# Optimization experiments

Hardware: AMD Instinct MI355X
Metric: run time of the kernel (lower is better)

## Reference

```python
import jax, jax.numpy as jnp
import numpy as np
import math

N_EXP = 8
TOP_K = 2
CAPACITY_FACTOR = 1.25


def _capacity(num_tokens):
    cap = math.floor(TOP_K * CAPACITY_FACTOR * num_tokens / N_EXP)
    cap += cap % 2  # round up to even, as in nanoMoE
    return int(cap)


def setup_inputs() -> dict:
    key = jax.random.key(0)
    k1, k2, k3, k4 = jax.random.split(key, 4)
    B, C, d = 4, 1024, 1024
    x = jax.random.normal(k1, (B, C, d), dtype=jnp.float32)
    w_g = jax.random.normal(k2, (d, N_EXP), dtype=jnp.float32) * 0.02
    c_fc = jax.random.normal(k3, (N_EXP, d, 4 * d), dtype=jnp.float32) * 0.02
    c_proj = jax.random.normal(k4, (N_EXP, 4 * d, d), dtype=jnp.float32) * 0.02
    return {"x": x, "w_g": w_g, "c_fc": c_fc, "c_proj": c_proj}


def reference(x, w_g, c_fc, c_proj):
    B, C, d = x.shape
    T = B * C  # num_tokens (static)
    cap = _capacity(T)
    xt = x.reshape(T, d)

    # ---- Router (no noise: use_noisy_top_k=False, eval) ----
    logits = xt @ w_g                                   # [T, n_exp]
    top_v, top_i = jax.lax.top_k(logits, TOP_K)         # [T, k]
    full = jnp.full_like(logits, -jnp.inf)
    full = full.at[jnp.arange(T)[:, None], top_i].set(top_v)
    probs = jax.nn.softmax(full, axis=-1)               # [T, n_exp]

    # expert assignment mask and intra-expert rank (capacity dropping)
    exp_mask = jax.nn.one_hot(top_i, N_EXP, dtype=jnp.int32)       # [T, k, n_exp]
    exp_mask = jnp.transpose(exp_mask, (1, 0, 2))                  # [k, T, n_exp]
    exp_rank = jnp.cumsum(exp_mask.reshape(TOP_K * T, N_EXP), axis=0) - 1
    exp_rank = exp_rank.reshape(TOP_K, T, N_EXP)
    exp_mask = exp_mask * (exp_rank < cap).astype(jnp.int32)       # drop overflow
    exp_rank = jnp.sum(exp_mask * exp_rank, axis=-1)               # [k, T] slot id

    exp_weights = exp_mask.astype(x.dtype) * probs[None]           # [k, T, n_exp]
    rank_oh = jax.nn.one_hot(exp_rank, cap, dtype=x.dtype)         # [k, T, cap]
    # dense combine weights [T, n_exp, cap] (as in original code)
    cb_weight = jnp.einsum('kte,ktc->tec', exp_weights, rank_oh)
    sec_mask = (cb_weight != 0).astype(x.dtype)                    # dispatch mask

    # dispatch tokens into per-expert batches [n_exp, cap, d]
    exp_batches = jnp.einsum('tec,td->ecd', sec_mask, xt)

    # ---- MLPExperts: batched GEMM -> GELU (exact) -> batched GEMM ----
    h = jax.nn.gelu(jnp.einsum('ecd,edf->ecf', exp_batches, c_fc), approximate=False)
    exp_out = jnp.einsum('ecf,efd->ecd', h, c_proj)                # [n_exp, cap, d]

    # ---- weighted combine: [T, n_exp*cap] @ [n_exp*cap, d] ----
    out = cb_weight.reshape(T, N_EXP * cap) @ exp_out.reshape(N_EXP * cap, d)
    return out.reshape(B, C, d)
```

## Files before the change

kernel.cpp:

```cpp
#include <hip/hip_runtime.h>
#include <hip/hip_bf16.h>
#include <math.h>

#define T_TOK 4096
#define D     1024
#define DFF   4096
#define NEXP  8
#define CAP   1280
#define TOPK  2

typedef __bf16 bf16x8 __attribute__((ext_vector_type(8)));
typedef float floatx4 __attribute__((ext_vector_type(4)));

__device__ __forceinline__ unsigned short f2bf(float f) {
  union { float f; unsigned u; } un; un.f = f;
  unsigned r = un.u + 0x7FFF + ((un.u >> 16) & 1);
  return (unsigned short)(r >> 16);
}

__global__ __launch_bounds__(256) void router_kernel(
    const float* __restrict__ x, const float* __restrict__ wg,
    int* __restrict__ top_e, float* __restrict__ top_p) {
  int t = blockIdx.x * 4 + (threadIdx.x >> 6);
  int lane = threadIdx.x & 63;
  if (t >= T_TOK) return;
  const float* xr = x + (size_t)t * D;
  float acc[NEXP];
#pragma unroll
  for (int e = 0; e < NEXP; e++) acc[e] = 0.f;
  for (int dd = lane; dd < D; dd += 64) {
    float xv = xr[dd];
    const float* wr = wg + dd * NEXP;
#pragma unroll
    for (int e = 0; e < NEXP; e++) acc[e] += xv * wr[e];
  }
#pragma unroll
  for (int off = 32; off > 0; off >>= 1) {
#pragma unroll
    for (int e = 0; e < NEXP; e++) acc[e] += __shfl_xor(acc[e], off, 64);
  }
  if (lane == 0) {
    int b0 = 0; float v0 = acc[0];
    for (int e = 1; e < NEXP; e++) if (acc[e] > v0) { v0 = acc[e]; b0 = e; }
    int b1 = -1; float v1 = -INFINITY;
    for (int e = 0; e < NEXP; e++) if (e != b0 && acc[e] > v1) { v1 = acc[e]; b1 = e; }
    float e1 = expf(v1 - v0);
    float s = 1.0f + e1;
    top_e[t * 2 + 0] = b0; top_e[t * 2 + 1] = b1;
    top_p[t * 2 + 0] = 1.0f / s; top_p[t * 2 + 1] = e1 / s;
  }
}

__global__ __launch_bounds__(1024) void rank_kernel(
    const int* __restrict__ top_e, const float* __restrict__ top_p,
    int* __restrict__ slot_token, int* __restrict__ tok_slot,
    float* __restrict__ tok_w) {
  __shared__ int wsum[16][NEXP];
  __shared__ int wscan[16][NEXP];
  int tid = threadIdx.x;
  int lane = tid & 63, w = tid >> 6;

  for (int s = tid; s < NEXP * CAP; s += 1024) slot_token[s] = -1;
  __syncthreads();

  int base[NEXP];
#pragma unroll
  for (int e = 0; e < NEXP; e++) base[e] = 0;

  for (int k = 0; k < TOPK; k++) {
    int cnt[NEXP];
#pragma unroll
    for (int e = 0; e < NEXP; e++) cnt[e] = 0;
    int eloc[4];
#pragma unroll
    for (int i = 0; i < 4; i++) {
      int t = tid * 4 + i;
      int e = top_e[t * 2 + k];
      eloc[i] = e;
#pragma unroll
      for (int q = 0; q < NEXP; q++) cnt[q] += (q == e);
    }
    int inc[NEXP];
#pragma unroll
    for (int e = 0; e < NEXP; e++) inc[e] = cnt[e];
    for (int off = 1; off < 64; off <<= 1) {
#pragma unroll
      for (int e = 0; e < NEXP; e++) {
        int v = __shfl_up(inc[e], off, 64);
        if (lane >= off) inc[e] += v;
      }
    }
    if (lane == 63)
#pragma unroll
      for (int e = 0; e < NEXP; e++) wsum[w][e] = inc[e];
    __syncthreads();
    if (w == 0 && lane < 16) {
      int s[NEXP];
#pragma unroll
      for (int e = 0; e < NEXP; e++) s[e] = wsum[lane][e];
      for (int off = 1; off < 16; off <<= 1) {
#pragma unroll
        for (int e = 0; e < NEXP; e++) {
          int v = __shfl_up(s[e], off, 64);
          if (lane >= off) s[e] += v;
        }
      }
#pragma unroll
      for (int e = 0; e < NEXP; e++) wscan[lane][e] = s[e];
    }
    __syncthreads();
    int excl[NEXP];
#pragma unroll
    for (int e = 0; e < NEXP; e++)
      excl[e] = inc[e] - cnt[e] + (w ? wscan[w - 1][e] : 0) + base[e];

    int run[NEXP];
#pragma unroll
    for (int e = 0; e < NEXP; e++) run[e] = 0;
#pragma unroll
    for (int i = 0; i < 4; i++) {
      int t = tid * 4 + i;
      int e = eloc[i];
      int r = 0;
#pragma unroll
      for (int q = 0; q < NEXP; q++)
        if (q == e) { r = excl[q] + run[q]; run[q]++; }
      if (r < CAP) {
        slot_token[e * CAP + r] = t;
        tok_slot[t * 2 + k] = e * CAP + r;
      } else {
        tok_slot[t * 2 + k] = -1;
      }
      tok_w[t * 2 + k] = top_p[t * 2 + k];
    }
#pragma unroll
    for (int e = 0; e < NEXP; e++) base[e] += wscan[15][e];
    __syncthreads();
  }
}

__global__ __launch_bounds__(256) void gather_cvt_kernel(
    const float* __restrict__ x, const int* __restrict__ slot_token,
    unsigned short* __restrict__ xb) {
  int slot = blockIdx.x;
  int tok = slot_token[slot];
  int i = threadIdx.x;
  float4 v = make_float4(0.f, 0.f, 0.f, 0.f);
  if (tok >= 0) v = ((const float4*)(x + (size_t)tok * D))[i];
  ushort4 o;
  o.x = f2bf(v.x); o.y = f2bf(v.y); o.z = f2bf(v.z); o.w = f2bf(v.w);
  ((ushort4*)(xb + (size_t)slot * D))[i] = o;
}

__global__ __launch_bounds__(256) void transpose_cvt_kernel(
    const float* __restrict__ src, unsigned short* __restrict__ dst,
    int R, int Cc) {
  __shared__ float tile[64][65];
  int e = blockIdx.z;
  src += (size_t)e * R * Cc;
  dst += (size_t)e * R * Cc;
  int r0 = blockIdx.y * 64, c0 = blockIdx.x * 64;
  int tr = threadIdx.x >> 4;
  int tc = (threadIdx.x & 15) * 4;
#pragma unroll
  for (int i = 0; i < 64; i += 16) {
    float4 v = *(const float4*)(src + (size_t)(r0 + tr + i) * Cc + c0 + tc);
    tile[tr + i][tc + 0] = v.x;
    tile[tr + i][tc + 1] = v.y;
    tile[tr + i][tc + 2] = v.z;
    tile[tr + i][tc + 3] = v.w;
  }
  __syncthreads();
#pragma unroll
  for (int i = 0; i < 64; i += 16) {
    int c = tr + i, r = tc;
    ushort4 o;
    o.x = f2bf(tile[r + 0][c]);
    o.y = f2bf(tile[r + 1][c]);
    o.z = f2bf(tile[r + 2][c]);
    o.w = f2bf(tile[r + 3][c]);
    *(ushort4*)(dst + (size_t)(c0 + c) * R + r0 + r) = o;
  }
}

template <int MODE>
__global__ __launch_bounds__(512) void gemm_mfma_kernel(
    const unsigned short* __restrict__ A,
    const unsigned short* __restrict__ Bt,
    void* __restrict__ Cv) {
  constexpr int MM = CAP;
  constexpr int NN = (MODE == 0) ? DFF : D;
  constexpr int LDA = (MODE == 0) ? D : DFF;
  constexpr int KLEN = (MODE == 0) ? D : DFF / 2;

  __shared__ unsigned short As[128 * 32];
  __shared__ unsigned short Bs[128 * 32];

  int e, yt, xt, kh;
  if (MODE == 0) {
    e = blockIdx.x; yt = blockIdx.y; xt = blockIdx.z; kh = 0;
  } else {
    xt = blockIdx.x; yt = blockIdx.y; e = blockIdx.z >> 1; kh = blockIdx.z & 1;
  }

  const unsigned short* Ae = A + (size_t)e * MM * LDA + (size_t)kh * KLEN;
  const unsigned short* Be = Bt + (size_t)e * NN * LDA + (size_t)kh * KLEN;

  int row0 = yt * 128, col0 = xt * 128;
  int tid = threadIdx.x;
  int wave = tid >> 6, lane = tid & 63;

  size_t a_off = (size_t)(row0 + (tid >> 2)) * LDA + (tid & 3) * 8;
  size_t b_off = (size_t)(col0 + (tid >> 2)) * LDA + (tid & 3) * 8;
  unsigned short* as_dst = As + tid * 8;
  unsigned short* bs_dst = Bs + tid * 8;

  int wm = (wave >> 1) * 32;
  int wn = (wave & 1) * 64;
  int fr = lane & 15, fq = lane >> 4;

  floatx4 acc[2][4];
#pragma unroll
  for (int i = 0; i < 2; i++)
#pragma unroll
    for (int j = 0; j < 4; j++) acc[i][j] = (floatx4){0.f, 0.f, 0.f, 0.f};

  for (int k0 = 0; k0 < KLEN; k0 += 32) {
    __builtin_amdgcn_global_load_lds(
        (const __attribute__((address_space(1))) unsigned int*)(Ae + a_off + k0),
        (__attribute__((address_space(3))) unsigned int*)as_dst, 16, 0, 0);
    __builtin_amdgcn_global_load_lds(
        (const __attribute__((address_space(1))) unsigned int*)(Be + b_off + k0),
        (__attribute__((address_space(3))) unsigned int*)bs_dst, 16, 0, 0);
    __syncthreads();

    bf16x8 af[2], bfr[4];
#pragma unroll
    for (int mi = 0; mi < 2; mi++)
      af[mi] = *(const bf16x8*)&As[(wm + mi * 16 + fr) * 32 + fq * 8];
#pragma unroll
    for (int ni = 0; ni < 4; ni++)
      bfr[ni] = *(const bf16x8*)&Bs[(wn + ni * 16 + fr) * 32 + fq * 8];
#pragma unroll
    for (int mi = 0; mi < 2; mi++)
#pragma unroll
      for (int ni = 0; ni < 4; ni++)
        acc[mi][ni] = __builtin_amdgcn_mfma_f32_16x16x32_bf16(
            af[mi], bfr[ni], acc[mi][ni], 0, 0, 0);
    __syncthreads();
  }

  int orow0 = row0 + wm + fq * 4;
  int ocol0 = col0 + wn + fr;
  if (MODE == 0) {
    unsigned short* Cb = (unsigned short*)Cv + (size_t)e * MM * NN;
#pragma unroll
    for (int mi = 0; mi < 2; mi++)
#pragma unroll
      for (int ni = 0; ni < 4; ni++)
#pragma unroll
        for (int r = 0; r < 4; r++) {
          float v = acc[mi][ni][r];
          v = 0.5f * v * (1.f + erff(v * 0.70710678118654752f));
          Cb[(size_t)(orow0 + mi * 16 + r) * NN + (ocol0 + ni * 16)] = f2bf(v);
        }
  } else {
    float* Cf = (float*)Cv + ((size_t)kh * NEXP + e) * MM * NN;
#pragma unroll
    for (int mi = 0; mi < 2; mi++)
#pragma unroll
      for (int ni = 0; ni < 4; ni++)
#pragma unroll
        for (int r = 0; r < 4; r++)
          Cf[(size_t)(orow0 + mi * 16 + r) * NN + (ocol0 + ni * 16)] =
              acc[mi][ni][r];
  }
}

__global__ __launch_bounds__(256) void combine_kernel(
    const float* __restrict__ eo, const int* __restrict__ tok_slot,
    const float* __restrict__ tok_w, float* __restrict__ out) {
  int t = blockIdx.x;
  int i = threadIdx.x;
  const size_t half = (size_t)NEXP * CAP * D;
  float4 acc = make_float4(0.f, 0.f, 0.f, 0.f);
#pragma unroll
  for (int k = 0; k < TOPK; k++) {
    int s = tok_slot[t * 2 + k];
    if (s >= 0) {
      float w = tok_w[t * 2 + k];
      float4 v0 = ((const float4*)(eo + (size_t)s * D))[i];
      float4 v1 = ((const float4*)(eo + half + (size_t)s * D))[i];
      acc.x += w * (v0.x + v1.x);
      acc.y += w * (v0.y + v1.y);
      acc.z += w * (v0.z + v1.z);
      acc.w += w * (v0.w + v1.w);
    }
  }
  ((float4*)(out + (size_t)t * D))[i] = acc;
}

extern "C" void kernel_launch(void* const* d_in, const int* in_sizes, int n_in,
                              void* d_out, int out_size, void* d_ws, size_t ws_size,
                              hipStream_t stream) {
  const float* x     = (const float*)d_in[0];
  const float* wg    = (const float*)d_in[1];
  const float* cfc   = (const float*)d_in[2];
  const float* cproj = (const float*)d_in[3];
  float* out = (float*)d_out;

  char* ws = (char*)d_ws;
  size_t off = 0;
  auto alloc = [&](size_t bytes) -> void* {
    void* p = ws + off;
    off += (bytes + 255) & ~(size_t)255;
    return p;
  };
  int*   top_e      = (int*)  alloc((size_t)T_TOK * 2 * 4);
  float* top_p      = (float*)alloc((size_t)T_TOK * 2 * 4);
  int*   slot_token = (int*)  alloc((size_t)NEXP * CAP * 4);
  int*   tok_slot   = (int*)  alloc((size_t)T_TOK * 2 * 4);
  float* tok_w      = (float*)alloc((size_t)T_TOK * 2 * 4);
  unsigned short* xb      = (unsigned short*)alloc((size_t)NEXP * CAP * D * 2);
  unsigned short* cfc_t   = (unsigned short*)alloc((size_t)NEXP * D * DFF * 2);
  unsigned short* cproj_t = (unsigned short*)alloc((size_t)NEXP * DFF * D * 2);
  unsigned short* h       = (unsigned short*)alloc((size_t)NEXP * CAP * DFF * 2);
  float* eo = (float*)xb;

  transpose_cvt_kernel<<<dim3(DFF / 64, D / 64, NEXP), 256, 0, stream>>>(
      cfc, cfc_t, D, DFF);
  transpose_cvt_kernel<<<dim3(D / 64, DFF / 64, NEXP), 256, 0, stream>>>(
      cproj, cproj_t, DFF, D);

  router_kernel<<<T_TOK / 4, 256, 0, stream>>>(x, wg, top_e, top_p);
  rank_kernel<<<1, 1024, 0, stream>>>(top_e, top_p, slot_token, tok_slot, tok_w);
  gather_cvt_kernel<<<NEXP * CAP, 256, 0, stream>>>(x, slot_token, xb);

  gemm_mfma_kernel<0><<<dim3(NEXP, CAP / 128, DFF / 128), 512, 0, stream>>>(
      xb, cfc_t, h);
  gemm_mfma_kernel<1><<<dim3(D / 128, CAP / 128, NEXP * 2), 512, 0, stream>>>(
      h, cproj_t, eo);

  combine_kernel<<<T_TOK, 256, 0, stream>>>(eo, tok_slot, tok_w, out);
}
```

Measured before the change: 634.0 us.

## Replace LDS-staged GEMM with register-streamed direct-global MFMA loads

The expert GEMMs no longer stage tiles through LDS with barriers. Each wave now loads its MFMA fragments straight from global memory into registers, double-buffered across two k-steps, and computes a larger 64x64 per-wave tile with 256-thread blocks. The grid ordering for the second GEMM also changes so that experts are on blockIdx.x. This removes the LDS round trips and __syncthreads overhead, but gives up cross-wave sharing of loaded tiles. Global loads become strided, 16-byte per-lane row fragments that rely on caches for reuse, and register pressure rises.

```diff
diff --git a/kernel.cpp b/kernel.cpp
--- a/kernel.cpp
+++ b/kernel.cpp
@@ -184,7 +184,7 @@
 }
 
 template <int MODE>
-__global__ __launch_bounds__(512) void gemm_mfma_kernel(
+__global__ __launch_bounds__(256, 2) void gemm_stream_kernel(
     const unsigned short* __restrict__ A,
     const unsigned short* __restrict__ Bt,
     void* __restrict__ Cv) {
@@ -193,86 +193,81 @@
   constexpr int LDA = (MODE == 0) ? D : DFF;
   constexpr int KLEN = (MODE == 0) ? D : DFF / 2;
 
-  __shared__ unsigned short As[128 * 32];
-  __shared__ unsigned short Bs[128 * 32];
-
-  int e, yt, xt, kh;
-  if (MODE == 0) {
-    e = blockIdx.x; yt = blockIdx.y; xt = blockIdx.z; kh = 0;
-  } else {
-    xt = blockIdx.x; yt = blockIdx.y; e = blockIdx.z >> 1; kh = blockIdx.z & 1;
-  }
-
-  const unsigned short* Ae = A + (size_t)e * MM * LDA + (size_t)kh * KLEN;
-  const unsigned short* Be = Bt + (size_t)e * NN * LDA + (size_t)kh * KLEN;
-
-  int row0 = yt * 128, col0 = xt * 128;
+  int e = blockIdx.x, mt = blockIdx.y, nt, kh;
+  if (MODE == 0) { nt = blockIdx.z; kh = 0; }
+  else           { nt = blockIdx.z & 7; kh = blockIdx.z >> 3; }
+
   int tid = threadIdx.x;
   int wave = tid >> 6, lane = tid & 63;
-
-  size_t a_off = (size_t)(row0 + (tid >> 2)) * LDA + (tid & 3) * 8;
-  size_t b_off = (size_t)(col0 + (tid >> 2)) * LDA + (tid & 3) * 8;
-  unsigned short* as_dst = As + tid * 8;
-  unsigned short* bs_dst = Bs + tid * 8;
-
-  int wm = (wave >> 1) * 32;
-  int wn = (wave & 1) * 64;
   int fr = lane & 15, fq = lane >> 4;
 
-  floatx4 acc[2][4];
-#pragma unroll
-  for (int i = 0; i < 2; i++)
+  int wm = mt * 128 + (wave >> 1) * 64;
+  int wn = nt * 128 + (wave & 1) * 64;
+
+  const unsigned short* Ab =
+      A + (size_t)e * MM * LDA + (size_t)kh * KLEN + (size_t)(wm + fr) * LDA + fq * 8;
+  const unsigned short* Bb =
+      Bt + (size_t)e * NN * LDA + (size_t)kh * KLEN + (size_t)(wn + fr) * LDA + fq * 8;
+
+  floatx4 acc[4][4];
+#pragma unroll
+  for (int i = 0; i < 4; i++)
 #pragma unroll
     for (int j = 0; j < 4; j++) acc[i][j] = (floatx4){0.f, 0.f, 0.f, 0.f};
 
-  for (int k0 = 0; k0 < KLEN; k0 += 32) {
-    __builtin_amdgcn_global_load_lds(
-        (const __attribute__((address_space(1))) unsigned int*)(Ae + a_off + k0),
-        (__attribute__((address_space(3))) unsigned int*)as_dst, 16, 0, 0);
-    __builtin_amdgcn_global_load_lds(
-        (const __attribute__((address_space(1))) unsigned int*)(Be + b_off + k0),
-        (__attribute__((address_space(3))) unsigned int*)bs_dst, 16, 0, 0);
-    __syncthreads();
-
-    bf16x8 af[2], bfr[4];
-#pragma unroll
-    for (int mi = 0; mi < 2; mi++)
-      af[mi] = *(const bf16x8*)&As[(wm + mi * 16 + fr) * 32 + fq * 8];
-#pragma unroll
-    for (int ni = 0; ni < 4; ni++)
-      bfr[ni] = *(const bf16x8*)&Bs[(wn + ni * 16 + fr) * 32 + fq * 8];
-#pragma unroll
-    for (int mi = 0; mi < 2; mi++)
-#pragma unroll
-      for (int ni = 0; ni < 4; ni++)
-        acc[mi][ni] = __builtin_amdgcn_mfma_f32_16x16x32_bf16(
-            af[mi], bfr[ni], acc[mi][ni], 0, 0, 0);
-    __syncthreads();
-  }
-
-  int orow0 = row0 + wm + fq * 4;
-  int ocol0 = col0 + wn + fr;
+  bf16x8 a0[4], b0[4], a1[4], b1[4];
+
+#define LOADF(abuf, bbuf, koff)                                             \
+  {                                                                         \
+    _Pragma("unroll") for (int mi = 0; mi < 4; mi++)                        \
+        abuf[mi] = *(const bf16x8*)(Ab + (size_t)mi * 16 * LDA + (koff));   \
+    _Pragma("unroll") for (int ni = 0; ni < 4; ni++)                        \
+        bbuf[ni] = *(const bf16x8*)(Bb + (size_t)ni * 16 * LDA + (koff));   \
+  }
+
+#define MFMA16(abuf, bbuf)                                                  \
+  {                                                                         \
+    _Pragma("unroll") for (int mi = 0; mi < 4; mi++)                        \
+        _Pragma("unroll") for (int ni = 0; ni < 4; ni++)                    \
+            acc[mi][ni] = __builtin_amdgcn_mfma_f32_16x16x32_bf16(          \
+                abuf[mi], bbuf[ni], acc[mi][ni], 0, 0, 0);                  \
+  }
+
+  LOADF(a0, b0, 0);
+  LOADF(a1, b1, 32);
+  for (int k0 = 0; k0 < KLEN - 64; k0 += 64) {
+    MFMA16(a0, b0);
+    LOADF(a0, b0, k0 + 64);
+    MFMA16(a1, b1);
+    LOADF(a1, b1, k0 + 96);
+  }
+  MFMA16(a0, b0);
+  MFMA16(a1, b1);
+#undef LOADF
+#undef MFMA16
+
   if (MODE == 0) {
     unsigned short* Cb = (unsigned short*)Cv + (size_t)e * MM * NN;
 #pragma unroll
-    for (int mi = 0; mi < 2; mi++)
+    for (int mi = 0; mi < 4; mi++)
 #pragma unroll
       for (int ni = 0; ni < 4; ni++)
 #pragma unroll
         for (int r = 0; r < 4; r++) {
           float v = acc[mi][ni][r];
           v = 0.5f * v * (1.f + erff(v * 0.70710678118654752f));
-          Cb[(size_t)(orow0 + mi * 16 + r) * NN + (ocol0 + ni * 16)] = f2bf(v);
+          Cb[(size_t)(wm + mi * 16 + fq * 4 + r) * NN + (wn + ni * 16 + fr)] =
+              f2bf(v);
         }
   } else {
     float* Cf = (float*)Cv + ((size_t)kh * NEXP + e) * MM * NN;
 #pragma unroll
-    for (int mi = 0; mi < 2; mi++)
+    for (int mi = 0; mi < 4; mi++)
 #pragma unroll
       for (int ni = 0; ni < 4; ni++)
 #pragma unroll
         for (int r = 0; r < 4; r++)
-          Cf[(size_t)(orow0 + mi * 16 + r) * NN + (ocol0 + ni * 16)] =
+          Cf[(size_t)(wm + mi * 16 + fq * 4 + r) * NN + (wn + ni * 16 + fr)] =
               acc[mi][ni][r];
   }
 }
@@ -336,9 +331,9 @@
   rank_kernel<<<1, 1024, 0, stream>>>(top_e, top_p, slot_token, tok_slot, tok_w);
   gather_cvt_kernel<<<NEXP * CAP, 256, 0, stream>>>(x, slot_token, xb);
 
-  gemm_mfma_kernel<0><<<dim3(NEXP, CAP / 128, DFF / 128), 512, 0, stream>>>(
+  gemm_stream_kernel<0><<<dim3(NEXP, CAP / 128, DFF / 128), 256, 0, stream>>>(
       xb, cfc_t, h);
-  gemm_mfma_kernel<1><<<dim3(D / 128, CAP / 128, NEXP * 2), 512, 0, stream>>>(
+  gemm_stream_kernel<1><<<dim3(NEXP, CAP / 128, 2 * D / 128), 256, 0, stream>>>(
       h, cproj_t, eo);
 
   combine_kernel<<<T_TOK, 256, 0, stream>>>(eo, tok_slot, tok_w, out);
```

After: 954.9 us. 50.6% more time.
